# Kernel optimization log

Measured on AMD Instinct MI355X. Metric: run time of the kernel, lower is better.

## Reference

```python
import jax, jax.numpy as jnp
import numpy as np

NUM_POINTS = 2_000_000
N = 2_000_000

# SH constants (standard real spherical harmonics, as in gaussian-splatting)
C0 = 0.28209479177387814
C1 = 0.4886025119029199
C2 = (1.0925484305920792, -1.0925484305920792, 0.31539156525252005,
      -1.0925484305920792, 0.5462742152960396)
C3 = (-0.5900435899266435, 2.890611442640554, -0.4570457994644658,
      0.3731763325901154, -0.4570457994644658, 1.445305721320277,
      -0.5900435899266435)


def sh_basis_deg3(dirs):
    # dirs: [N,3] unit vectors -> basis [N,16]
    x, y, z = dirs[:, 0], dirs[:, 1], dirs[:, 2]
    xx, yy, zz = x * x, y * y, z * z
    xy, yz, xz = x * y, y * z, x * z
    one = jnp.ones_like(x)
    return jnp.stack([
        C0 * one,
        -C1 * y, C1 * z, -C1 * x,
        C2[0] * xy, C2[1] * yz, C2[2] * (2.0 * zz - xx - yy),
        C2[3] * xz, C2[4] * (xx - yy),
        C3[0] * y * (3.0 * xx - yy), C3[1] * xy * z,
        C3[2] * y * (4.0 * zz - xx - yy),
        C3[3] * z * (2.0 * zz - 3.0 * xx - 3.0 * yy),
        C3[4] * x * (4.0 * zz - xx - yy),
        C3[5] * z * (xx - yy), C3[6] * x * (xx - yy),
    ], axis=-1)


def setup_inputs() -> dict:
    key = jax.random.key(0)
    ks = jax.random.split(key, 8)
    return {
        "positions": jax.random.normal(ks[0], (N, 3), jnp.float32),
        "indexes": jax.random.randint(ks[1], (N,), 0, NUM_POINTS, jnp.int64)
            if jax.config.jax_enable_x64 else
            jax.random.randint(ks[1], (N,), 0, NUM_POINTS, jnp.int32),
        "cam_pos": jax.random.normal(ks[2], (3,), jnp.float32),
        "glo_feature": jax.random.normal(ks[3], (1, 16), jnp.float32),
        "base_sh": jax.random.normal(ks[4], (NUM_POINTS, 3, 1), jnp.float32),
        "higher_sh": jnp.zeros((NUM_POINTS, 3, 15), jnp.float32)
            + 0.01 * jax.random.normal(ks[5], (NUM_POINTS, 3, 15), jnp.float32),
        "w1": jax.random.normal(ks[6], (16, 32), jnp.float32) * (1.0 / np.sqrt(16)),
        "b1": jnp.zeros((32,), jnp.float32),
        "ln_w": jnp.ones((32,), jnp.float32),
        "ln_b": jnp.zeros((32,), jnp.float32),
        "w2": jax.random.normal(ks[7], (32, 12), jnp.float32) * (1.0 / np.sqrt(32)),
        "b2": jnp.zeros((12,), jnp.float32),
    }


def mlp(glo, w1, b1, ln_w, ln_b, w2, b2, out_scale=1e-12):
    h = glo @ w1 + b1                      # [1,32]
    mu = jnp.mean(h, axis=-1, keepdims=True)
    var = jnp.mean((h - mu) ** 2, axis=-1, keepdims=True)
    h = (h - mu) * jax.lax.rsqrt(var + 1e-5) * ln_w + ln_b
    h = jax.nn.relu(h)
    return (h @ w2 + b2) * out_scale       # [1,12]


def reference(positions, indexes, cam_pos, glo_feature, base_sh, higher_sh,
              w1, b1, ln_w, ln_b, w2, b2):
    sh_features = jnp.concatenate([base_sh, higher_sh], axis=2)  # [P,3,16]
    sh = sh_features[indexes]                                    # gather [N,3,16]
    dirs = positions - cam_pos
    dirs = dirs / jnp.linalg.norm(dirs, axis=-1, keepdims=True)
    basis = sh_basis_deg3(dirs)                                  # [N,16]
    colors = jnp.einsum('nck,nk->nc', sh, basis) + 0.5           # [N,3]
    colors4 = jnp.concatenate([colors, jnp.ones_like(colors[:, :1])], axis=1)  # [N,4]
    affine_res = mlp(glo_feature, w1, b1, ln_w, ln_b, w2, b2).reshape(1, 3, 4)
    affine = affine_res + jnp.eye(3, 4, dtype=jnp.float32)[None]  # [1,3,4]
    out = jnp.einsum('nj,ij->ni', colors4, affine[0])             # [N,3]
    return jnp.clip(out, 0.0, 1.0), jnp.mean(jnp.abs(affine_res))
```

## Files before the change

kernel.cpp:

```cpp
#include <hip/hip_runtime.h>
#include <math.h>


__global__ void mlp_prologue_kernel(const float* __restrict__ glo,
                                    const float* __restrict__ w1,
                                    const float* __restrict__ b1,
                                    const float* __restrict__ ln_w,
                                    const float* __restrict__ ln_b,
                                    const float* __restrict__ w2,
                                    const float* __restrict__ b2,
                                    float* __restrict__ affine_out,
                                    float* __restrict__ mean_out)
{
    float h[32];
    #pragma unroll
    for (int j = 0; j < 32; ++j) {
        float s = b1[j];
        #pragma unroll
        for (int k = 0; k < 16; ++k) s += glo[k] * w1[k * 32 + j];
        h[j] = s;
    }
    float mu = 0.f;
    #pragma unroll
    for (int j = 0; j < 32; ++j) mu += h[j];
    mu *= (1.f / 32.f);
    float var = 0.f;
    #pragma unroll
    for (int j = 0; j < 32; ++j) { float d = h[j] - mu; var += d * d; }
    var *= (1.f / 32.f);
    float inv = rsqrtf(var + 1e-5f);
    #pragma unroll
    for (int j = 0; j < 32; ++j) {
        float v = (h[j] - mu) * inv * ln_w[j] + ln_b[j];
        h[j] = v > 0.f ? v : 0.f;
    }
    float sabs = 0.f;
    #pragma unroll
    for (int i = 0; i < 12; ++i) {
        float s = b2[i];
        #pragma unroll
        for (int j = 0; j < 32; ++j) s += h[j] * w2[j * 12 + i];
        s *= 1e-12f;
        sabs += fabsf(s);
        float e = ((i & 3) == (i >> 2)) ? 1.f : 0.f;
        affine_out[i] = s + e;
    }
    *mean_out = sabs * (1.f / 12.f);
}

__global__ __launch_bounds__(256) void transfer_sh_kernel(
    const float* __restrict__ positions,
    const int*   __restrict__ indexes,
    const float* __restrict__ cam_pos,
    const float* __restrict__ base_sh,
    const float* __restrict__ higher_sh,
    const float* __restrict__ affine,
    float* __restrict__ out,
    int n)
{
    int i = blockIdx.x * blockDim.x + threadIdx.x;
    if (i >= n) return;

    float px = positions[3 * i + 0] - cam_pos[0];
    float py = positions[3 * i + 1] - cam_pos[1];
    float pz = positions[3 * i + 2] - cam_pos[2];
    float rn = rsqrtf(px * px + py * py + pz * pz);
    float x = px * rn, y = py * rn, z = pz * rn;

    float xx = x * x, yy = y * y, zz = z * z;
    float xy = x * y, yz = y * z, xz = x * z;

    float b[16];
    b[0]  = 0.28209479177387814f;
    b[1]  = -0.4886025119029199f * y;
    b[2]  =  0.4886025119029199f * z;
    b[3]  = -0.4886025119029199f * x;
    b[4]  =  1.0925484305920792f * xy;
    b[5]  = -1.0925484305920792f * yz;
    b[6]  =  0.31539156525252005f * (2.f * zz - xx - yy);
    b[7]  = -1.0925484305920792f * xz;
    b[8]  =  0.5462742152960396f * (xx - yy);
    b[9]  = -0.5900435899266435f * y * (3.f * xx - yy);
    b[10] =  2.890611442640554f  * xy * z;
    b[11] = -0.4570457994644658f * y * (4.f * zz - xx - yy);
    b[12] =  0.3731763325901154f * z * (2.f * zz - 3.f * xx - 3.f * yy);
    b[13] = -0.4570457994644658f * x * (4.f * zz - xx - yy);
    b[14] =  1.445305721320277f  * z * (xx - yy);
    b[15] = -0.5900435899266435f * x * (xx - yy);

    long idx = (long)indexes[i];
    const float* bs = base_sh + 3 * idx;
    const float* hs = higher_sh + 45 * idx;

    float c[3];
    #pragma unroll
    for (int ch = 0; ch < 3; ++ch) {
        float s = bs[ch] * b[0];
        #pragma unroll
        for (int k = 0; k < 15; ++k) s += hs[ch * 15 + k] * b[k + 1];
        c[ch] = s + 0.5f;
    }

    #pragma unroll
    for (int r = 0; r < 3; ++r) {
        float v = c[0] * affine[4 * r + 0] + c[1] * affine[4 * r + 1] +
                  c[2] * affine[4 * r + 2] + affine[4 * r + 3];
        v = fminf(fmaxf(v, 0.f), 1.f);
        out[3 * i + r] = v;
    }
}

extern "C" void kernel_launch(void* const* d_in, const int* in_sizes, int n_in,
                              void* d_out, int out_size, void* d_ws, size_t ws_size,
                              hipStream_t stream) {
    const float* positions = (const float*)d_in[0];
    const int*   indexes   = (const int*)d_in[1];
    const float* cam_pos   = (const float*)d_in[2];
    const float* glo       = (const float*)d_in[3];
    const float* base_sh   = (const float*)d_in[4];
    const float* higher_sh = (const float*)d_in[5];
    const float* w1        = (const float*)d_in[6];
    const float* b1        = (const float*)d_in[7];
    const float* ln_w      = (const float*)d_in[8];
    const float* ln_b      = (const float*)d_in[9];
    const float* w2        = (const float*)d_in[10];
    const float* b2        = (const float*)d_in[11];

    float* out    = (float*)d_out;
    float* affine = (float*)d_ws;

    int n = in_sizes[0] / 3;
    float* mean_out = out + (out_size - 1);

    mlp_prologue_kernel<<<1, 1, 0, stream>>>(glo, w1, b1, ln_w, ln_b, w2, b2,
                                             affine, mean_out);

    int block = 256;
    int grid = (n + block - 1) / block;
    transfer_sh_kernel<<<grid, block, 0, stream>>>(positions, indexes, cam_pos,
                                                   base_sh, higher_sh, affine,
                                                   out, n);
}
```

Measured before the change: 598.8 us.

## Vectorize higher_sh gather with aligned float4 loads and parallelize MLP prologue

The per-point gather of 45 higher-order SH coefficients is replaced by twelve aligned float4 loads covering the 48-float window, and a switch on the misalignment offset selects which floats feed the dot products. This cuts the number of scalar gather instructions per thread. The single-thread MLP prologue becomes a 64-thread kernel that uses wavefront shuffles for the layer-norm reductions, shortening the serial launch ahead of the main kernel. The aligned window can read up to three floats past the row, including past the end of the buffer for the last point. The four-way switch may also raise register pressure or cause divergence.

```diff
diff --git a/kernel.cpp b/kernel.cpp
--- a/kernel.cpp
+++ b/kernel.cpp
@@ -2,50 +2,60 @@
 #include <math.h>
 
 
-__global__ void mlp_prologue_kernel(const float* __restrict__ glo,
-                                    const float* __restrict__ w1,
-                                    const float* __restrict__ b1,
-                                    const float* __restrict__ ln_w,
-                                    const float* __restrict__ ln_b,
-                                    const float* __restrict__ w2,
-                                    const float* __restrict__ b2,
-                                    float* __restrict__ affine_out,
-                                    float* __restrict__ mean_out)
+__global__ __launch_bounds__(64) void mlp_prologue_kernel(
+    const float* __restrict__ glo,
+    const float* __restrict__ w1,
+    const float* __restrict__ b1,
+    const float* __restrict__ ln_w,
+    const float* __restrict__ ln_b,
+    const float* __restrict__ w2,
+    const float* __restrict__ b2,
+    float* __restrict__ affine_out,
+    float* __restrict__ mean_out)
 {
-    float h[32];
+    __shared__ float hsh[32];
+    __shared__ float ssh[12];
+    int t = threadIdx.x;
+
+    float h = 0.f;
+    if (t < 32) {
+        h = b1[t];
+        #pragma unroll
+        for (int k = 0; k < 16; ++k) h += glo[k] * w1[k * 32 + t];
+    }
+    float s = h;
     #pragma unroll
-    for (int j = 0; j < 32; ++j) {
-        float s = b1[j];
+    for (int off = 32; off > 0; off >>= 1) s += __shfl_down(s, off);
+    float mu = __shfl(s, 0) * (1.f / 32.f);
+
+    float d = (t < 32) ? (h - mu) : 0.f;
+    float v2 = d * d;
+    #pragma unroll
+    for (int off = 32; off > 0; off >>= 1) v2 += __shfl_down(v2, off);
+    float var = __shfl(v2, 0) * (1.f / 32.f);
+    float inv = rsqrtf(var + 1e-5f);
+
+    if (t < 32) {
+        float v = (h - mu) * inv * ln_w[t] + ln_b[t];
+        hsh[t] = v > 0.f ? v : 0.f;
+    }
+    __syncthreads();
+    if (t < 12) {
+        float s2 = b2[t];
         #pragma unroll
-        for (int k = 0; k < 16; ++k) s += glo[k] * w1[k * 32 + j];
-        h[j] = s;
+        for (int j = 0; j < 32; ++j) s2 += hsh[j] * w2[j * 12 + t];
+        s2 *= 1e-12f;
+        ssh[t] = fabsf(s2);
+        float e = ((t & 3) == (t >> 2)) ? 1.f : 0.f;
+        affine_out[t] = s2 + e;
     }
-    float mu = 0.f;
-    #pragma unroll
-    for (int j = 0; j < 32; ++j) mu += h[j];
-    mu *= (1.f / 32.f);
-    float var = 0.f;
-    #pragma unroll
-    for (int j = 0; j < 32; ++j) { float d = h[j] - mu; var += d * d; }
-    var *= (1.f / 32.f);
-    float inv = rsqrtf(var + 1e-5f);
-    #pragma unroll
-    for (int j = 0; j < 32; ++j) {
-        float v = (h[j] - mu) * inv * ln_w[j] + ln_b[j];
-        h[j] = v > 0.f ? v : 0.f;
+    __syncthreads();
+    if (t == 0) {
+        float sa = 0.f;
+        #pragma unroll
+        for (int i = 0; i < 12; ++i) sa += ssh[i];
+        *mean_out = sa * (1.f / 12.f);
     }
-    float sabs = 0.f;
-    #pragma unroll
-    for (int i = 0; i < 12; ++i) {
-        float s = b2[i];
-        #pragma unroll
-        for (int j = 0; j < 32; ++j) s += h[j] * w2[j * 12 + i];
-        s *= 1e-12f;
-        sabs += fabsf(s);
-        float e = ((i & 3) == (i >> 2)) ? 1.f : 0.f;
-        affine_out[i] = s + e;
-    }
-    *mean_out = sabs * (1.f / 12.f);
 }
 
 __global__ __launch_bounds__(256) void transfer_sh_kernel(
@@ -71,7 +81,6 @@
     float xy = x * y, yz = y * z, xz = x * z;
 
     float b[16];
-    b[0]  = 0.28209479177387814f;
     b[1]  = -0.4886025119029199f * y;
     b[2]  =  0.4886025119029199f * z;
     b[3]  = -0.4886025119029199f * x;
@@ -88,25 +97,51 @@
     b[14] =  1.445305721320277f  * z * (xx - yy);
     b[15] = -0.5900435899266435f * x * (xx - yy);
 
-    long idx = (long)indexes[i];
-    const float* bs = base_sh + 3 * idx;
-    const float* hs = higher_sh + 45 * idx;
+    unsigned idx = (unsigned)indexes[i];
 
-    float c[3];
+    float a0 = base_sh[3 * idx + 0];
+    float a1 = base_sh[3 * idx + 1];
+    float a2 = base_sh[3 * idx + 2];
+    const float C0 = 0.28209479177387814f;
+    float c0 = a0 * C0 + 0.5f;
+    float c1 = a1 * C0 + 0.5f;
+    float c2 = a2 * C0 + 0.5f;
+
+    unsigned fo = 45u * idx;
+    const float4* W = (const float4*)(higher_sh + (fo & ~3u));
+    float4 v[12];
     #pragma unroll
-    for (int ch = 0; ch < 3; ++ch) {
-        float s = bs[ch] * b[0];
-        #pragma unroll
-        for (int k = 0; k < 15; ++k) s += hs[ch * 15 + k] * b[k + 1];
-        c[ch] = s + 0.5f;
+    for (int q = 0; q < 12; ++q) v[q] = W[q];
+    float Wf[48];
+    #pragma unroll
+    for (int q = 0; q < 12; ++q) {
+        Wf[4 * q + 0] = v[q].x; Wf[4 * q + 1] = v[q].y;
+        Wf[4 * q + 2] = v[q].z; Wf[4 * q + 3] = v[q].w;
     }
+
+#define ACC(M)                                      \
+    {                                               \
+        _Pragma("unroll")                           \
+        for (int k = 0; k < 15; ++k) {              \
+            c0 += Wf[(M) + k]      * b[k + 1];      \
+            c1 += Wf[(M) + 15 + k] * b[k + 1];      \
+            c2 += Wf[(M) + 30 + k] * b[k + 1];      \
+        }                                           \
+    }
+    switch (fo & 3u) {
+        case 0: ACC(0) break;
+        case 1: ACC(1) break;
+        case 2: ACC(2) break;
+        default: ACC(3) break;
+    }
+#undef ACC
 
     #pragma unroll
     for (int r = 0; r < 3; ++r) {
-        float v = c[0] * affine[4 * r + 0] + c[1] * affine[4 * r + 1] +
-                  c[2] * affine[4 * r + 2] + affine[4 * r + 3];
-        v = fminf(fmaxf(v, 0.f), 1.f);
-        out[3 * i + r] = v;
+        float vv = c0 * affine[4 * r + 0] + c1 * affine[4 * r + 1] +
+                   c2 * affine[4 * r + 2] + affine[4 * r + 3];
+        vv = fminf(fmaxf(vv, 0.f), 1.f);
+        out[3 * i + r] = vv;
     }
 }
 
@@ -132,8 +167,8 @@
     int n = in_sizes[0] / 3;
     float* mean_out = out + (out_size - 1);
 
-    mlp_prologue_kernel<<<1, 1, 0, stream>>>(glo, w1, b1, ln_w, ln_b, w2, b2,
-                                             affine, mean_out);
+    mlp_prologue_kernel<<<1, 64, 0, stream>>>(glo, w1, b1, ln_w, ln_b, w2, b2,
+                                              affine, mean_out);
 
     int block = 256;
     int grid = (n + block - 1) / block;
```

Result: faster. 578.6 us (-3.4%).
